# Kernel tuning notes

Hardware: AMD Instinct MI355X
Metric: run time of the kernel (lower is better)

Reference implementation:

```python
import jax, jax.numpy as jnp
import numpy as np
import math

DIM = 1024
HEADS = 16
WINDOW = 256  # window_size; also used as block size (band covers 3 blocks)


def _rope(x):
    # canonical half-split RoPE over the FULL feature dim (as the module applies
    # it before the head split), base 10000
    b, s, d = x.shape
    half = d // 2
    inv_freq = 1.0 / (10000.0 ** (jnp.arange(half, dtype=jnp.float32) / half))
    ang = jnp.arange(s, dtype=jnp.float32)[:, None] * inv_freq[None, :]  # [s, half]
    cos, sin = jnp.cos(ang), jnp.sin(ang)
    x1, x2 = x[..., :half], x[..., half:]
    return jnp.concatenate([x1 * cos - x2 * sin, x1 * sin + x2 * cos], axis=-1)


def setup_inputs() -> dict:
    key = jax.random.key(0)
    ks = jax.random.split(key, 8)
    d = DIM
    q = jax.random.normal(ks[0], (2, 4096, d), dtype=jnp.float32)
    k = jax.random.normal(ks[1], (2, 4096, d), dtype=jnp.float32)
    v = jax.random.normal(ks[2], (2, 4096, d), dtype=jnp.float32)
    wq = jax.random.normal(ks[3], (d, d), dtype=jnp.float32) * 0.02
    wk = jax.random.normal(ks[4], (d, d), dtype=jnp.float32) * 0.02
    wv = jax.random.normal(ks[5], (d, d), dtype=jnp.float32) * 0.02
    wo_w = jax.random.normal(ks[6], (d, d), dtype=jnp.float32) * 0.02
    wo_b = jnp.zeros((d,), dtype=jnp.float32)
    return {"q": q, "k": k, "v": v, "wq": wq, "wk": wk, "wv": wv,
            "wo_w": wo_w, "wo_b": wo_b}


def reference(q, k, v, wq, wk, wv, wo_w, wo_b):
    b, s, d = q.shape
    h, W = HEADS, WINDOW
    dk = d // h
    B = W                      # block size == window -> band of 3 blocks
    nb = s // B

    # projections (torch Linear: x @ W^T), then RoPE over the full dim
    qp = _rope(jnp.einsum('bsd,ed->bse', q, wq))
    kp = _rope(jnp.einsum('bsd,ed->bse', k, wk))
    vp = jnp.einsum('bsd,ed->bse', v, wv)

    # split heads -> [b, h, s, dk]
    qh = qp.reshape(b, s, h, dk).transpose(0, 2, 1, 3)
    kh = kp.reshape(b, s, h, dk).transpose(0, 2, 1, 3)
    vh = vp.reshape(b, s, h, dk).transpose(0, 2, 1, 3)

    # pad keys/values by one block on each side, gather 3-block bands
    kpad = jnp.pad(kh, ((0, 0), (0, 0), (B, B), (0, 0)))
    vpad = jnp.pad(vh, ((0, 0), (0, 0), (B, B), (0, 0)))
    kblk = kpad.reshape(b, h, nb + 2, B, dk)
    vblk = vpad.reshape(b, h, nb + 2, B, dk)
    kband = jnp.concatenate([kblk[:, :, i:i + nb] for i in range(3)], axis=3)  # [b,h,nb,3B,dk]
    vband = jnp.concatenate([vblk[:, :, i:i + nb] for i in range(3)], axis=3)

    qb = qh.reshape(b, h, nb, B, dk)
    # NOTE: original multiplies by sqrt(dim_k) (not divides) -- kept faithfully
    scores = jnp.einsum('bhnqd,bhnkd->bhnqk', qb, kband) * math.sqrt(dk)

    # band mask: key global pos = (n-1)*B + ki, query global pos = n*B + qi
    n_idx = jnp.arange(nb)[:, None, None]
    qi = jnp.arange(B)[None, :, None]
    ki = jnp.arange(3 * B)[None, None, :]
    kpos = (n_idx - 1) * B + ki
    rel = ki - B - qi  # key_pos - query_pos
    valid = (rel >= -W) & (rel <= W) & (kpos >= 0) & (kpos < s)  # [nb,B,3B]

    neg = jnp.asarray(jnp.finfo(scores.dtype).min, scores.dtype)
    scores = jnp.where(valid[None, None], scores, neg)
    attn = jax.nn.softmax(scores, axis=-1)

    out = jnp.einsum('bhnqk,bhnkd->bhnqd', attn, vband)
    out = out.reshape(b, h, s, dk).transpose(0, 2, 1, 3).reshape(b, s, d)
    return jnp.einsum('bsd,ed->bse', out, wo_w) + wo_b
```

## Files before the change

kernel.cpp:

```cpp
#include <hip/hip_runtime.h>


typedef __attribute__((ext_vector_type(8))) short short8v;
typedef __attribute__((ext_vector_type(4))) float float4v;
typedef __attribute__((ext_vector_type(8))) _Float16 half8v;

#define MFMA_BF16(A_, B_, C_) __builtin_amdgcn_mfma_f32_16x16x32_bf16((A_), (B_), (C_), 0, 0, 0)
#define MFMA_F16(A_, B_, C_)  __builtin_amdgcn_mfma_f32_16x16x32_f16((A_), (B_), (C_), 0, 0, 0)

#define VMW_(n) asm volatile("s_waitcnt vmcnt(" #n ")" ::: "memory")
#define VMW(n) VMW_(n)
#define LGKM0 asm volatile("s_waitcnt lgkmcnt(0)" ::: "memory")
#define BARF do { __builtin_amdgcn_s_barrier(); asm volatile("" ::: "memory"); } while (0)
#define FENCE asm volatile("" ::: "memory")

__device__ __forceinline__ void split_rn(float x, short& h, short& l) {
    unsigned int u = __float_as_uint(x);
    u += 0x7fffu + ((u >> 16) & 1u);
    unsigned int hb = u & 0xffff0000u;
    h = (short)(hb >> 16);
    float lo = x - __uint_as_float(hb);
    l = (short)(__float_as_uint(lo) >> 16);
}

__device__ __forceinline__ void dma16(const void* g, void* l) {
    __builtin_amdgcn_global_load_lds(
        (__attribute__((address_space(1))) void*)g,
        (__attribute__((address_space(3))) void*)l, 16, 0, 0);
}

__global__ __launch_bounds__(256) void prep_k(
    const float* __restrict__ wq, const float* __restrict__ wk,
    const float* __restrict__ wv, unsigned short* __restrict__ scr)
{
    const int M1 = 1 << 20;
    unsigned int tid = blockIdx.x * 256 + threadIdx.x;
    if (tid < (unsigned)M1) {
        short h, l; split_rn(wq[tid], h, l);
        scr[tid] = (unsigned short)h;
        scr[M1 + tid] = (unsigned short)l;
    } else if (tid < (unsigned)(2 * M1)) {
        unsigned int i = tid - M1;
        short h, l; split_rn(wk[i], h, l);
        scr[2 * M1 + i] = (unsigned short)h;
        scr[3 * M1 + i] = (unsigned short)l;
    } else {
        unsigned int i = tid - 2 * M1;
        scr[4 * M1 + i] = __builtin_bit_cast(unsigned short, (_Float16)wv[i]);
    }
}

__global__ __launch_bounds__(512, 2) void gemm_qk2(
    const float* __restrict__ A0, const short* __restrict__ Bh0,
    const short* __restrict__ Bl0, float* __restrict__ C0,
    const float* __restrict__ A1, const short* __restrict__ Bh1,
    const short* __restrict__ Bl1, float* __restrict__ C1)
{
    __shared__ __align__(16) short S[2 * 32768];

    const int bid = blockIdx.x;
    const int cid = ((bid & 7) << 5) | (bid >> 3);
    const int z   = cid >> 7;
    const int rem = cid & 127;
    const int bm  = (rem >> 2) << 8;
    const int bn  = (rem & 3) << 8;

    const float* Ap  = z ? A1  : A0;
    const short* Bhp = z ? Bh1 : Bh0;
    const short* Blp = z ? Bl1 : Bl0;
    float*       Cp  = z ? C1  : C0;

    const int t = threadIdx.x;
    const int wave = t >> 6, lane = t & 63;
    const int c16 = lane & 15, quad = lane >> 4;
    const int wm = (wave >> 2) << 7;
    const int wn = (wave & 3) << 6;

    const int ar = t >> 1;
    const int ah16 = (t & 1) << 4;
    const int fA = (ar & 3) ^ ((ar >> 2) & 3);
    const int swA0 = ((((t & 1) << 1) | 0) ^ fA) << 3;
    const int swA1 = ((((t & 1) << 1) | 1) ^ fA) << 3;

    const int br  = lane >> 2;
    const int fsl = (((lane & 3) ^ ((br & 3) ^ ((br >> 2) & 3))) << 3);

    const int frd = ((quad ^ ((c16 & 3) ^ ((c16 >> 2) & 3))) << 3);

    float4v acc[8][4];
#pragma unroll
    for (int i = 0; i < 8; i++)
#pragma unroll
        for (int j = 0; j < 4; j++) acc[i][j] = (float4v){0.f, 0.f, 0.f, 0.f};

#define STAGE_B(pp, kk)                                                          \
    do {                                                                         \
        const size_t rb = (size_t)(bn + (wave << 5) + br) * 1024 + (kk) + fsl;   \
        short* dh = S + (pp) * 32768 + 16384 + (wave << 10);                     \
        short* dl = dh + 8192;                                                   \
        dma16(Bhp + rb,             dh);                                         \
        dma16(Bhp + rb + 16 * 1024, dh + 512);                                   \
        dma16(Blp + rb,             dl);                                         \
        dma16(Blp + rb + 16 * 1024, dl + 512);                                   \
    } while (0)

#define SPLIT_WRITE(sp_)                                                         \
    do {                                                                         \
        short8v h0, l0, h1, l1;                                                  \
        _Pragma("unroll")                                                        \
        for (int jj = 0; jj < 4; jj++) {                                         \
            short hh, ll;                                                        \
            split_rn(ap0[jj], hh, ll); h0[jj] = hh;     l0[jj] = ll;             \
            split_rn(ap1[jj], hh, ll); h0[jj + 4] = hh; l0[jj + 4] = ll;         \
            split_rn(ap2[jj], hh, ll); h1[jj] = hh;     l1[jj] = ll;             \
            split_rn(ap3[jj], hh, ll); h1[jj + 4] = hh; l1[jj + 4] = ll;         \
        }                                                                        \
        short* abase = (sp_) + ar * 32;                                          \
        *(short8v*)(abase + swA0) = h0;                                          \
        *(short8v*)(abase + swA1) = h1;                                          \
        *(short8v*)(abase + 8192 + swA0) = l0;                                   \
        *(short8v*)(abase + 8192 + swA1) = l1;                                   \
    } while (0)

#define MFMA_CLUSTER(AARR, BARR)                                                 \
    do {                                                                         \
        __builtin_amdgcn_s_setprio(1);                                           \
        _Pragma("unroll")                                                        \
        for (int i = 0; i < 8; i++)                                              \
            _Pragma("unroll")                                                    \
            for (int j = 0; j < 4; j++)                                          \
                acc[i][j] = MFMA_BF16(AARR[i & 7], BARR[j & 3], acc[i][j]);      \
        __builtin_amdgcn_s_setprio(0);                                           \
    } while (0)

    const float* arow = Ap + (size_t)(bm + ar) * 1024 + ah16;
    float4v ap0 = *(const float4v*)(arow + 0);
    float4v ap1 = *(const float4v*)(arow + 4);
    float4v ap2 = *(const float4v*)(arow + 8);
    float4v ap3 = *(const float4v*)(arow + 12);
    FENCE;
    STAGE_B(0, 0);
    VMW(4);
    SPLIT_WRITE(S);
    FENCE;
    ap0 = *(const float4v*)(arow + 32);
    ap1 = *(const float4v*)(arow + 36);
    ap2 = *(const float4v*)(arow + 40);
    ap3 = *(const float4v*)(arow + 44);
    LGKM0;

    int kb = 0;
#pragma unroll 1
    for (int tt = 0; tt < 31; ++tt, kb += 32) {
        short* sp = S + (tt & 1) * 32768;
        short* sn = S + ((tt & 1) ^ 1) * 32768;

        STAGE_B((tt & 1) ^ 1, kb + 32);
        VMW(8);
        BARF;

        short8v ahv[8], bhv[4];
#pragma unroll
        for (int i = 0; i < 8; i++)
            ahv[i] = *(const short8v*)(sp + (wm + i * 16 + c16) * 32 + frd);
#pragma unroll
        for (int j = 0; j < 4; j++)
            bhv[j] = *(const short8v*)(sp + 16384 + (wn + j * 16 + c16) * 32 + frd);
        MFMA_CLUSTER(ahv, bhv);

        {
            short8v blv[4];
#pragma unroll
            for (int j = 0; j < 4; j++)
                blv[j] = *(const short8v*)(sp + 24576 + (wn + j * 16 + c16) * 32 + frd);
            MFMA_CLUSTER(ahv, blv);
        }

        VMW(4);
        SPLIT_WRITE(sn);
        FENCE;
        {
            int kn = kb + 64;
            if (kn >= 1024) kn = 0;
            ap0 = *(const float4v*)(arow + kn);
            ap1 = *(const float4v*)(arow + kn + 4);
            ap2 = *(const float4v*)(arow + kn + 8);
            ap3 = *(const float4v*)(arow + kn + 12);
        }

        {
            short8v alv[8];
#pragma unroll
            for (int i = 0; i < 8; i++)
                alv[i] = *(const short8v*)(sp + 8192 + (wm + i * 16 + c16) * 32 + frd);
            MFMA_CLUSTER(alv, bhv);
        }
        LGKM0;
        BARF;
    }

    {
        short* sp = S + 32768;
        VMW(4);
        BARF;
        short8v ahv[8], bhv[4];
#pragma unroll
        for (int i = 0; i < 8; i++)
            ahv[i] = *(const short8v*)(sp + (wm + i * 16 + c16) * 32 + frd);
#pragma unroll
        for (int j = 0; j < 4; j++)
            bhv[j] = *(const short8v*)(sp + 16384 + (wn + j * 16 + c16) * 32 + frd);
        MFMA_CLUSTER(ahv, bhv);
        {
            short8v blv[4];
#pragma unroll
            for (int j = 0; j < 4; j++)
                blv[j] = *(const short8v*)(sp + 24576 + (wn + j * 16 + c16) * 32 + frd);
            MFMA_CLUSTER(ahv, blv);
        }
        {
            short8v alv[8];
#pragma unroll
            for (int i = 0; i < 8; i++)
                alv[i] = *(const short8v*)(sp + 8192 + (wm + i * 16 + c16) * 32 + frd);
            MFMA_CLUSTER(alv, bhv);
        }
    }

#undef STAGE_B
#undef SPLIT_WRITE
#undef MFMA_CLUSTER

#pragma unroll
    for (int i = 0; i < 8; i++) {
        const size_t gr0 = (size_t)(bm + wm + i * 16 + quad * 4);
#pragma unroll
        for (int j = 0; j < 4; j++) {
            const int gc = bn + wn + j * 16 + c16;
#pragma unroll
            for (int r = 0; r < 4; r++)
                Cp[(gr0 + r) * 1024 + gc] = acc[i][j][r];
        }
    }
}

template <int AF16, int BF16, int OMODE>
__global__ __launch_bounds__(256) void gemm16(
    const void* __restrict__ Ap, const void* __restrict__ Bp,
    void* __restrict__ Cp, const float* __restrict__ bias)
{
    const int N = 1024, K = 1024;

    __shared__ __align__(16) short As[128 * 32];
    __shared__ __align__(16) short Bs[128 * 32];

    const int t = threadIdx.x;
    const int bm = blockIdx.y << 7;
    const int bn = blockIdx.x << 7;
    const int lane = t & 63;
    const int wave = t >> 6;
    const int wm = (wave >> 1) << 6;
    const int wn = (wave & 1) << 6;
    const int c16 = lane & 15;
    const int quad = lane >> 4;
    const int lr = t >> 2;
    const int lc = (t & 3) << 3;

    float4v acc[4][4];
#pragma unroll
    for (int i = 0; i < 4; i++)
#pragma unroll
        for (int j = 0; j < 4; j++) acc[i][j] = (float4v){0.f, 0.f, 0.f, 0.f};

    for (int kb = 0; kb < K; kb += 32) {
        if (AF16) {
            const _Float16* Af = (const _Float16*)Ap;
#pragma unroll
            for (int g = 0; g < 2; g++)
                dma16(Af + (size_t)(bm + g * 64 + lr) * K + kb + lc,
                      As + g * 2048 + wave * 512);
        } else {
            const float* Af = (const float*)Ap;
#pragma unroll
            for (int g = 0; g < 2; g++) {
                const float* src = Af + (size_t)(bm + g * 64 + lr) * K + kb + lc;
                float4v f0 = *(const float4v*)src;
                float4v f1 = *(const float4v*)(src + 4);
                half8v h;
#pragma unroll
                for (int j = 0; j < 8; j++) h[j] = (_Float16)((j < 4) ? f0[j] : f1[j - 4]);
                *(half8v*)(As + (g * 64 + lr) * 32 + lc) = h;
            }
        }
        if (BF16) {
            const _Float16* Bf = (const _Float16*)Bp;
#pragma unroll
            for (int g = 0; g < 2; g++)
                dma16(Bf + (size_t)(bn + g * 64 + lr) * K + kb + lc,
                      Bs + g * 2048 + wave * 512);
        } else {
            const float* Bf = (const float*)Bp;
#pragma unroll
            for (int g = 0; g < 2; g++) {
                const float* src = Bf + (size_t)(bn + g * 64 + lr) * K + kb + lc;
                float4v f0 = *(const float4v*)src;
                float4v f1 = *(const float4v*)(src + 4);
                half8v h;
#pragma unroll
                for (int j = 0; j < 8; j++) h[j] = (_Float16)((j < 4) ? f0[j] : f1[j - 4]);
                *(half8v*)(Bs + (g * 64 + lr) * 32 + lc) = h;
            }
        }
        __syncthreads();

        half8v ah[4], bh[4];
#pragma unroll
        for (int i = 0; i < 4; i++)
            ah[i] = *(const half8v*)(As + (wm + i * 16 + c16) * 32 + quad * 8);
#pragma unroll
        for (int j = 0; j < 4; j++)
            bh[j] = *(const half8v*)(Bs + (wn + j * 16 + c16) * 32 + quad * 8);
#pragma unroll
        for (int i = 0; i < 4; i++)
#pragma unroll
            for (int j = 0; j < 4; j++)
                acc[i][j] = MFMA_F16(ah[i], bh[j], acc[i][j]);
        __syncthreads();
    }

#pragma unroll
    for (int i = 0; i < 4; i++)
#pragma unroll
        for (int j = 0; j < 4; j++)
#pragma unroll
            for (int r = 0; r < 4; r++) {
                int gr = bm + wm + i * 16 + quad * 4 + r;
                int gc = bn + wn + j * 16 + c16;
                float vv = acc[i][j][r];
                if (OMODE == 0) {
                    ((unsigned short*)Cp)[((size_t)(gc << 1) + (gr >> 12)) * 4096 + (gr & 4095)] =
                        __builtin_bit_cast(unsigned short, (_Float16)vv);
                } else {
                    ((float*)Cp)[(size_t)gr * N + gc] = vv + bias[gc];
                }
            }
}

__global__ __launch_bounds__(256) void rope_pack(float* __restrict__ QP, float* __restrict__ KP)
{
    int sp = blockIdx.x;
    int t = threadIdx.x;
    float* rows[4] = { QP + ((size_t)sp << 10), QP + ((size_t)(4096 + sp) << 10),
                       KP + ((size_t)sp << 10), KP + ((size_t)(4096 + sp) << 10) };

    float c[2], sn[2];
    float x1[4][2], x2[4][2];
#pragma unroll
    for (int p = 0; p < 2; p++) {
        int j = t + p * 256;
        float freq = __expf(-0.017988946f * (float)j);
        float ang = (float)sp * freq;
        sincosf(ang, &sn[p], &c[p]);
#pragma unroll
        for (int r = 0; r < 4; r++) {
            x1[r][p] = rows[r][j];
            x2[r][p] = rows[r][j + 512];
        }
    }
    __syncthreads();
#pragma unroll
    for (int r = 0; r < 4; r++) {
        unsigned short* u = (unsigned short*)rows[r];
#pragma unroll
        for (int p = 0; p < 2; p++) {
            int j = t + p * 256;
            float y1 = x1[r][p] * c[p] - x2[r][p] * sn[p];
            float y2 = x1[r][p] * sn[p] + x2[r][p] * c[p];
            short h1, l1, h2, l2;
            split_rn(y1, h1, l1);
            split_rn(y2, h2, l2);
            u[j] = (unsigned short)h1;
            u[j + 512] = (unsigned short)h2;
            u[1024 + j] = (unsigned short)l1;
            u[1024 + j + 512] = (unsigned short)l2;
        }
    }
}

__global__ __launch_bounds__(256) void attn_k(
    const unsigned short* __restrict__ QHL, const unsigned short* __restrict__ KHL,
    const unsigned short* __restrict__ VT, unsigned short* __restrict__ AO)
{
    const int S = 4096;
    const float NEG = -1e30f;
    const float PSC = 512.0f;
    const int bq = blockIdx.x, h = blockIdx.y, b = blockIdx.z;
    const int t = threadIdx.x;
    const int wave = t >> 6, lane = t & 63;
    const int col = lane & 15, quad = lane >> 4;
    const int qg = (bq << 6) + (wave << 4);

    __shared__ __align__(16) short Khs[64 * 72];
    __shared__ __align__(16) short Kls[64 * 72];
    __shared__ __align__(16) short Vs[64 * 72];
    __shared__ __align__(16) short Ps[4][16 * 72];
    short* myP = &Ps[wave][0];

    const int sk = t >> 3;
    const int sd = (t & 7) << 3;

    short8v qh[2], ql[2];
    {
        const unsigned short* qr = QHL + ((size_t)(b * S + qg + col) << 11) + h * 64 + quad * 8;
        qh[0] = *(const short8v*)(qr);
        qh[1] = *(const short8v*)(qr + 32);
        ql[0] = *(const short8v*)(qr + 1024);
        ql[1] = *(const short8v*)(qr + 1024 + 32);
    }

    float mrun[4], lrun[4];
    float4v O[4];
#pragma unroll
    for (int r = 0; r < 4; r++) { mrun[r] = NEG; lrun[r] = 0.f; }
#pragma unroll
    for (int t4 = 0; t4 < 4; t4++) O[t4] = (float4v){0.f, 0.f, 0.f, 0.f};

    const int blk0 = bq << 6;
    const int kstart = (blk0 - 256 > 0) ? (blk0 - 256) : 0;
    const int kend = (blk0 + 320 < S) ? (blk0 + 320) : S;

    for (int kb = kstart; kb < kend; kb += 64) {
#pragma unroll
        for (int p = 0; p < 2; p++) {
            int key = p * 32 + sk;
            const unsigned short* krow = KHL + ((size_t)(b * S + kb + key) << 11) + h * 64 + sd;
            *(short8v*)(Khs + key * 72 + sd) = *(const short8v*)krow;
            *(short8v*)(Kls + key * 72 + sd) = *(const short8v*)(krow + 1024);
            int dm = p * 32 + sk;
            const unsigned short* vrow = VT + ((size_t)((h * 64 + dm) << 1) + b) * S + kb + sd;
            *(short8v*)(Vs + dm * 72 + sd) = *(const short8v*)vrow;
        }
        __syncthreads();

        float4v sv[4];
#pragma unroll
        for (int c = 0; c < 4; c++) {
            const short* kro = Khs + (c * 16 + col) * 72 + quad * 8;
            const short* klo = Kls + (c * 16 + col) * 72 + quad * 8;
            short8v kh0 = *(const short8v*)kro;
            short8v kh1 = *(const short8v*)(kro + 32);
            short8v kl0 = *(const short8v*)klo;
            short8v kl1 = *(const short8v*)(klo + 32);
            float4v sc = (float4v){0.f, 0.f, 0.f, 0.f};
            sc = MFMA_BF16(qh[0], kh0, sc);
            sc = MFMA_BF16(qh[1], kh1, sc);
            sc = MFMA_BF16(qh[0], kl0, sc);
            sc = MFMA_BF16(qh[1], kl1, sc);
            sc = MFMA_BF16(ql[0], kh0, sc);
            sc = MFMA_BF16(ql[1], kh1, sc);
            sv[c] = sc;
        }

        float mx[4], alpha[4], psum[4];
#pragma unroll
        for (int r = 0; r < 4; r++) {
            int qrow = qg + quad * 4 + r;
            float m = NEG;
#pragma unroll
            for (int c = 0; c < 4; c++) {
                int key = kb + c * 16 + col;
                float vv = (key >= qrow - 256 && key <= qrow + 256) ? sv[c][r] * 8.0f : NEG;
                sv[c][r] = vv;
                m = fmaxf(m, vv);
            }
            mx[r] = m;
        }
#pragma unroll
        for (int st = 1; st < 16; st <<= 1)
#pragma unroll
            for (int r = 0; r < 4; r++) mx[r] = fmaxf(mx[r], __shfl_xor(mx[r], st, 64));

#pragma unroll
        for (int r = 0; r < 4; r++) {
            float mn = fmaxf(mrun[r], mx[r]);
            alpha[r] = __expf(mrun[r] - mn);
            mrun[r] = mn;
            float ps = 0.f;
#pragma unroll
            for (int c = 0; c < 4; c++) {
                float p = __expf(sv[c][r] - mn);
                ps += p;
                myP[(quad * 4 + r) * 72 + c * 16 + col] =
                    __builtin_bit_cast(short, (_Float16)(p * PSC));
            }
            psum[r] = ps;
        }
#pragma unroll
        for (int st = 1; st < 16; st <<= 1)
#pragma unroll
            for (int r = 0; r < 4; r++) psum[r] += __shfl_xor(psum[r], st, 64);
#pragma unroll
        for (int r = 0; r < 4; r++) lrun[r] = lrun[r] * alpha[r] + psum[r];
#pragma unroll
        for (int t4 = 0; t4 < 4; t4++)
#pragma unroll
            for (int r = 0; r < 4; r++) O[t4][r] *= alpha[r];

#pragma unroll
        for (int kf = 0; kf < 2; kf++) {
            half8v pa = *(const half8v*)(myP + col * 72 + kf * 32 + quad * 8);
#pragma unroll
            for (int t4 = 0; t4 < 4; t4++) {
                half8v vb = *(const half8v*)(Vs + (t4 * 16 + col) * 72 + kf * 32 + quad * 8);
                O[t4] = MFMA_F16(pa, vb, O[t4]);
            }
        }
        __syncthreads();
    }

#pragma unroll
    for (int r = 0; r < 4; r++) {
        float inv = (lrun[r] > 0.f) ? (1.0f / (lrun[r] * PSC)) : 0.f;
        unsigned short* orow = AO + (size_t)(b * S + qg + quad * 4 + r) * 1024 + h * 64;
#pragma unroll
        for (int t4 = 0; t4 < 4; t4++)
            orow[t4 * 16 + col] = __builtin_bit_cast(unsigned short, (_Float16)(O[t4][r] * inv));
    }
}

extern "C" void kernel_launch(void* const* d_in, const int* in_sizes, int n_in,
                              void* d_out, int out_size, void* d_ws, size_t ws_size,
                              hipStream_t stream) {
    const float* q   = (const float*)d_in[0];
    const float* k   = (const float*)d_in[1];
    const float* v   = (const float*)d_in[2];
    const float* wq  = (const float*)d_in[3];
    const float* wk  = (const float*)d_in[4];
    const float* wv  = (const float*)d_in[5];
    const float* wo  = (const float*)d_in[6];
    const float* wob = (const float*)d_in[7];

    float* QP = (float*)d_ws;
    float* KP = QP + (size_t)8192 * 1024;
    unsigned short* VT = (unsigned short*)(KP + (size_t)8192 * 1024);
    unsigned short* AO = VT + (size_t)8192 * 1024;

    unsigned short* scr = (unsigned short*)d_out;
    const int M1 = 1 << 20;
    const short* wqh = (const short*)(scr);
    const short* wql = (const short*)(scr + M1);
    const short* wkh = (const short*)(scr + 2 * M1);
    const short* wkl = (const short*)(scr + 3 * M1);
    const void*  wv16 = (const void*)(scr + 4 * M1);

    prep_k<<<12288, 256, 0, stream>>>(wq, wk, wv, scr);
    gemm_qk2<<<256, 512, 0, stream>>>(q, wqh, wql, QP, k, wkh, wkl, KP);
    rope_pack<<<4096, 256, 0, stream>>>(QP, KP);
    gemm16<0, 1, 0><<<dim3(8, 64), 256, 0, stream>>>(v, wv16, (void*)VT, nullptr);
    attn_k<<<dim3(64, 16, 2), 256, 0, stream>>>((const unsigned short*)QP,
                                                (const unsigned short*)KP, VT, AO);
    gemm16<1, 0, 1><<<dim3(8, 64), 256, 0, stream>>>(AO, wo, d_out, wob);
}
```

Before: 419.1 us.

## Double-buffer attention K/V tiles with async DMA, larger blocks, and skip unneeded masking

Restructures the banded attention kernel: 128 queries per 512-thread block, K/V tiles double-buffered in LDS via async global-to-LDS copies with an XOR swizzle instead of padding, and MFMA sections wrapped in raised wave priority. The band mask is applied only on edge tiles, rescaling of O and l happens only when the running max grows, and the sqrt(dk) factor of 8 is folded into Q during RoPE packing. This targets load latency and per-tile softmax overhead, at the cost of more LDS per block and reliance on a dma16 helper defined elsewhere.

```diff
diff --git a/kernel.cpp b/kernel.cpp
--- a/kernel.cpp
+++ b/kernel.cpp
@@ -371,11 +371,12 @@
 #pragma unroll
     for (int r = 0; r < 4; r++) {
         unsigned short* u = (unsigned short*)rows[r];
+        const float sc8 = (r < 2) ? 8.0f : 1.0f;
 #pragma unroll
         for (int p = 0; p < 2; p++) {
             int j = t + p * 256;
-            float y1 = x1[r][p] * c[p] - x2[r][p] * sn[p];
-            float y2 = x1[r][p] * sn[p] + x2[r][p] * c[p];
+            float y1 = (x1[r][p] * c[p] - x2[r][p] * sn[p]) * sc8;
+            float y2 = (x1[r][p] * sn[p] + x2[r][p] * c[p]) * sc8;
             short h1, l1, h2, l2;
             split_rn(y1, h1, l1);
             split_rn(y2, h2, l2);
@@ -387,7 +388,7 @@
     }
 }
 
-__global__ __launch_bounds__(256) void attn_k(
+__global__ __launch_bounds__(512, 4) void attn_k(
     const unsigned short* __restrict__ QHL, const unsigned short* __restrict__ KHL,
     const unsigned short* __restrict__ VT, unsigned short* __restrict__ AO)
 {
@@ -398,16 +399,28 @@
     const int t = threadIdx.x;
     const int wave = t >> 6, lane = t & 63;
     const int col = lane & 15, quad = lane >> 4;
-    const int qg = (bq << 6) + (wave << 4);
-
-    __shared__ __align__(16) short Khs[64 * 72];
-    __shared__ __align__(16) short Kls[64 * 72];
-    __shared__ __align__(16) short Vs[64 * 72];
-    __shared__ __align__(16) short Ps[4][16 * 72];
+    const int qg = (bq << 7) + (wave << 4);
+
+    __shared__ __align__(16) short Khs[2][64 * 64];
+    __shared__ __align__(16) short Kls[2][64 * 64];
+    __shared__ __align__(16) short Vs [2][64 * 64];
+    __shared__ __align__(16) short Ps[8][16 * 72];
     short* myP = &Ps[wave][0];
 
-    const int sk = t >> 3;
-    const int sd = (t & 7) << 3;
+    const int rg = lane >> 3;
+    const int ch = (((lane & 7) ^ rg) << 3);
+    const int srow = (wave << 3) + rg;
+
+    const unsigned short* kbase = KHL + ((size_t)(b * S + srow) << 11) + h * 64 + ch;
+    const unsigned short* vbase = VT + ((size_t)((h * 64 + srow) << 1) + b) * S + ch;
+
+#define STAGE(pp, kk)                                          \
+    do {                                                       \
+        const unsigned short* kr = kbase + ((size_t)(kk) << 11); \
+        dma16(kr,        &Khs[pp][wave << 9]);                 \
+        dma16(kr + 1024, &Kls[pp][wave << 9]);                 \
+        dma16(vbase + (kk), &Vs[pp][wave << 9]);               \
+    } while (0)
 
     short8v qh[2], ql[2];
     {
@@ -418,39 +431,43 @@
         ql[1] = *(const short8v*)(qr + 1024 + 32);
     }
 
-    float mrun[4], lrun[4];
+    float mrun[4], lrun[4], psum[4];
     float4v O[4];
 #pragma unroll
     for (int r = 0; r < 4; r++) { mrun[r] = NEG; lrun[r] = 0.f; }
 #pragma unroll
     for (int t4 = 0; t4 < 4; t4++) O[t4] = (float4v){0.f, 0.f, 0.f, 0.f};
 
-    const int blk0 = bq << 6;
+    const int blk0 = bq << 7;
     const int kstart = (blk0 - 256 > 0) ? (blk0 - 256) : 0;
-    const int kend = (blk0 + 320 < S) ? (blk0 + 320) : S;
-
-    for (int kb = kstart; kb < kend; kb += 64) {
-#pragma unroll
-        for (int p = 0; p < 2; p++) {
-            int key = p * 32 + sk;
-            const unsigned short* krow = KHL + ((size_t)(b * S + kb + key) << 11) + h * 64 + sd;
-            *(short8v*)(Khs + key * 72 + sd) = *(const short8v*)krow;
-            *(short8v*)(Kls + key * 72 + sd) = *(const short8v*)(krow + 1024);
-            int dm = p * 32 + sk;
-            const unsigned short* vrow = VT + ((size_t)((h * 64 + dm) << 1) + b) * S + kb + sd;
-            *(short8v*)(Vs + dm * 72 + sd) = *(const short8v*)vrow;
-        }
-        __syncthreads();
-
+    const int kend = (blk0 + 384 < S) ? (blk0 + 384) : S;
+    const int nt = (kend - kstart) >> 6;
+
+    STAGE(0, kstart);
+
+#pragma unroll 1
+    for (int it = 0; it < nt; ++it) {
+        const int kb = kstart + (it << 6);
+        const int p = it & 1;
+        if (it + 1 < nt) { STAGE(p ^ 1, kb + 64); VMW(3); }
+        else             { VMW(0); }
+        BARF;
+
+        const short* KHp = &Khs[p][0];
+        const short* KLp = &Kls[p][0];
         float4v sv[4];
+        __builtin_amdgcn_s_setprio(1);
 #pragma unroll
         for (int c = 0; c < 4; c++) {
-            const short* kro = Khs + (c * 16 + col) * 72 + quad * 8;
-            const short* klo = Kls + (c * 16 + col) * 72 + quad * 8;
-            short8v kh0 = *(const short8v*)kro;
-            short8v kh1 = *(const short8v*)(kro + 32);
-            short8v kl0 = *(const short8v*)klo;
-            short8v kl1 = *(const short8v*)(klo + 32);
+            const int row = c * 16 + col;
+            const int c0 = ((quad ^ (col & 7)) << 3);
+            const int c1 = (((quad + 4) ^ (col & 7)) << 3);
+            const short* kro = KHp + (row << 6);
+            const short* klo = KLp + (row << 6);
+            short8v kh0 = *(const short8v*)(kro + c0);
+            short8v kh1 = *(const short8v*)(kro + c1);
+            short8v kl0 = *(const short8v*)(klo + c0);
+            short8v kl1 = *(const short8v*)(klo + c1);
             float4v sc = (float4v){0.f, 0.f, 0.f, 0.f};
             sc = MFMA_BF16(qh[0], kh0, sc);
             sc = MFMA_BF16(qh[1], kh1, sc);
@@ -460,63 +477,79 @@
             sc = MFMA_BF16(ql[1], kh1, sc);
             sv[c] = sc;
         }
-
-        float mx[4], alpha[4], psum[4];
+        __builtin_amdgcn_s_setprio(0);
+
+        const bool masked = (kb < blk0 - 128) || (kb > blk0 + 192);
+        float mx[4];
+        if (masked) {
+#pragma unroll
+            for (int r = 0; r < 4; r++) {
+                int qrow = qg + quad * 4 + r;
+                float m = NEG;
+#pragma unroll
+                for (int c = 0; c < 4; c++) {
+                    int key = kb + c * 16 + col;
+                    float vv = (key >= qrow - 256 && key <= qrow + 256) ? sv[c][r] : NEG;
+                    sv[c][r] = vv;
+                    m = fmaxf(m, vv);
+                }
+                mx[r] = m;
+            }
+        } else {
+#pragma unroll
+            for (int r = 0; r < 4; r++)
+                mx[r] = fmaxf(fmaxf(sv[0][r], sv[1][r]), fmaxf(sv[2][r], sv[3][r]));
+        }
+#pragma unroll
+        for (int st = 1; st < 16; st <<= 1)
+#pragma unroll
+            for (int r = 0; r < 4; r++) mx[r] = fmaxf(mx[r], __shfl_xor(mx[r], st, 64));
+
 #pragma unroll
         for (int r = 0; r < 4; r++) {
-            int qrow = qg + quad * 4 + r;
-            float m = NEG;
+            if (mx[r] > mrun[r]) {
+                float al = __expf(mrun[r] - mx[r]);
+                mrun[r] = mx[r];
+                lrun[r] *= al;
+#pragma unroll
+                for (int t4 = 0; t4 < 4; t4++) O[t4][r] *= al;
+            }
+            float mn = mrun[r];
+            float ps = 0.f;
 #pragma unroll
             for (int c = 0; c < 4; c++) {
-                int key = kb + c * 16 + col;
-                float vv = (key >= qrow - 256 && key <= qrow + 256) ? sv[c][r] * 8.0f : NEG;
-                sv[c][r] = vv;
-                m = fmaxf(m, vv);
-            }
-            mx[r] = m;
+                float pv = __expf(sv[c][r] - mn);
+                ps += pv;
+                myP[(quad * 4 + r) * 72 + c * 16 + col] =
+                    __builtin_bit_cast(short, (_Float16)(pv * PSC));
+            }
+            psum[r] = ps;
         }
 #pragma unroll
         for (int st = 1; st < 16; st <<= 1)
 #pragma unroll
-            for (int r = 0; r < 4; r++) mx[r] = fmaxf(mx[r], __shfl_xor(mx[r], st, 64));
-
-#pragma unroll
-        for (int r = 0; r < 4; r++) {
-            float mn = fmaxf(mrun[r], mx[r]);
-            alpha[r] = __expf(mrun[r] - mn);
-            mrun[r] = mn;
-            float ps = 0.f;
-#pragma unroll
-            for (int c = 0; c < 4; c++) {
-                float p = __expf(sv[c][r] - mn);
-                ps += p;
-                myP[(quad * 4 + r) * 72 + c * 16 + col] =
-                    __builtin_bit_cast(short, (_Float16)(p * PSC));
-            }
-            psum[r] = ps;
-        }
-#pragma unroll
-        for (int st = 1; st < 16; st <<= 1)
-#pragma unroll
             for (int r = 0; r < 4; r++) psum[r] += __shfl_xor(psum[r], st, 64);
 #pragma unroll
-        for (int r = 0; r < 4; r++) lrun[r] = lrun[r] * alpha[r] + psum[r];
-#pragma unroll
-        for (int t4 = 0; t4 < 4; t4++)
-#pragma unroll
-            for (int r = 0; r < 4; r++) O[t4][r] *= alpha[r];
-
+        for (int r = 0; r < 4; r++) lrun[r] += psum[r];
+
+        const short* Vp = &Vs[p][0];
+        __builtin_amdgcn_s_setprio(1);
 #pragma unroll
         for (int kf = 0; kf < 2; kf++) {
             half8v pa = *(const half8v*)(myP + col * 72 + kf * 32 + quad * 8);
 #pragma unroll
             for (int t4 = 0; t4 < 4; t4++) {
-                half8v vb = *(const half8v*)(Vs + (t4 * 16 + col) * 72 + kf * 32 + quad * 8);
+                const int vrow = t4 * 16 + col;
+                const int vc = ((((kf << 2) + quad) ^ (col & 7)) << 3);
+                half8v vb = *(const half8v*)(Vp + (vrow << 6) + vc);
                 O[t4] = MFMA_F16(pa, vb, O[t4]);
             }
         }
-        __syncthreads();
-    }
+        __builtin_amdgcn_s_setprio(0);
+
+        BARF;
+    }
+#undef STAGE
 
 #pragma unroll
     for (int r = 0; r < 4; r++) {
@@ -554,10 +587,10 @@
     const void*  wv16 = (const void*)(scr + 4 * M1);
 
     prep_k<<<12288, 256, 0, stream>>>(wq, wk, wv, scr);
-    gemm_qk2<<<256, 512, 0, stream>>>(q, wqh, wql, QP, k, wkh, wkl, KP);
+    gemm_qk2<<<dim3(256), 512, 0, stream>>>(q, wqh, wql, QP, k, wkh, wkl, KP);
     rope_pack<<<4096, 256, 0, stream>>>(QP, KP);
     gemm16<0, 1, 0><<<dim3(8, 64), 256, 0, stream>>>(v, wv16, (void*)VT, nullptr);
-    attn_k<<<dim3(64, 16, 2), 256, 0, stream>>>((const unsigned short*)QP,
+    attn_k<<<dim3(32, 16, 2), 512, 0, stream>>>((const unsigned short*)QP,
                                                 (const unsigned short*)KP, VT, AO);
     gemm16<1, 0, 1><<<dim3(8, 64), 256, 0, stream>>>(AO, wo, d_out, wob);
 }
```

Measured after the change: 411.8 us. About the same (-1.7%).
